# Kernel optimization log

Measured on AMD Instinct MI355X. Metric: run time of the kernel, lower is better.

## Reference

```python
import jax, jax.numpy as jnp
import numpy as np

R0 = 1.0
DIM_A, DIM_V, DIM_D = 32, 32, 32
N_NODES = 20000
N_EDGES = 640000


def radial_encode_8(r, r0):
    # 8 Gaussian radial basis functions on the edge length |r_ij|
    d = jnp.linalg.norm(r, axis=-1)                      # [E]
    centers = jnp.linspace(0.0, r0, 8)                   # [8]
    width = r0 / 8.0
    return jnp.exp(-(((d[..., None] - centers) / width) ** 2))  # [E,8]


def tens_sigmoid_vec(v):
    # norm-saturating nonlinearity for rank-1 tensors (direction-preserving)
    n2 = jnp.sum(v * v, axis=-1, keepdims=True)
    return v * jax.lax.rsqrt(1.0 + n2)


def setup_inputs() -> dict:
    key = jax.random.key(0)
    ks = jax.random.split(key, 12)

    def lin(k, fan_in, fan_out):
        return jax.random.normal(k, (fan_in, fan_out), jnp.float32) / np.float32(np.sqrt(fan_in))

    return dict(
        r_ij=jax.random.normal(ks[0], (N_EDGES, 3), jnp.float32),
        w_rad=lin(ks[1], 8, DIM_A), b_rad=jnp.zeros((DIM_A,), jnp.float32),
        w_direct=lin(ks[2], DIM_A, DIM_A),
        w1=lin(ks[3], DIM_A, 2 * DIM_A), b1=jnp.zeros((2 * DIM_A,), jnp.float32),
        w2=lin(ks[4], 2 * DIM_A, 2 * DIM_A), b2=jnp.zeros((2 * DIM_A,), jnp.float32),
        w3=lin(ks[5], 2 * DIM_A, DIM_A), b3=jnp.zeros((DIM_A,), jnp.float32),
        w_v=lin(ks[6], DIM_A, DIM_V),
        w_d=lin(ks[7], DIM_A, DIM_D),
        edges_src=jax.random.randint(ks[8], (N_EDGES,), 0, N_NODES),
        n_nodes=N_NODES,
    )


def reference(r_ij, w_rad, b_rad, w_direct, w1, b1, w2, b2, w3, b3, w_v, w_d,
              edges_src, n_nodes):
    lrelu = lambda x: jnp.where(x > 0, x, 0.1 * x)
    # radial MLP: Linear(8, a) -> MLP (lin_direct + 3-layer leakyrelu net)
    h = radial_encode_8(r_ij, R0) @ w_rad + b_rad                      # [E,a]
    rad = h @ w_direct + (lrelu(lrelu(h @ w1 + b1) @ w2 + b2) @ w3 + b3)  # [E,a]
    rs = tens_sigmoid_vec(r_ij * (7.0 / R0))                            # [E,3]

    seg = lambda x: jax.ops.segment_sum(x, edges_src, num_segments=n_nodes)
    A_a = seg(rad)                                                      # [N,a]
    A_v = seg(rad[:, :, None] * rs[:, None, :])                         # [N,a,3]
    # phi_d_ij = rad ⊗ rs ⊗ rs per edge  -> [E,a,3,3], then scatter-sum
    A_d = seg(rad[:, :, None, None] * rs[:, None, None, :] * rs[:, None, :, None])  # [N,a,3,3]

    out_v = jnp.einsum('nac,av->nvc', A_v, w_v)                         # TensLinear rank 1
    out_d = jnp.einsum('naij,ad->ndij', A_d, w_d)                       # TensLinear rank 2
    return A_a, out_v, out_d
```

## Files before the change

kernel.cpp:

```cpp
#include <hip/hip_runtime.h>
#include <hip/hip_bf16.h>
#include <hip/hip_fp16.h>
#include <math.h>


#define TSIZE 8192
#define DMAX  2.0f
#define NPB   4
#define EPB   4

#define O_WRAD 0
#define O_BRAD 256
#define O_WDIR 288
#define O_W1   1312
#define O_B1   3360
#define O_W2   3424
#define O_B2   7520
#define O_W3   7584
#define O_B3   9632
#define O_WV   9664
#define O_WD   10688
#define W_TOT  11712

__device__ __forceinline__ float lrelu(float x) { return x > 0.0f ? x : 0.1f * x; }

__device__ __forceinline__ float ldf(const void* p, int i, bool f32) {
    return f32 ? ((const float*)p)[i]
               : __uint_as_float(((unsigned int)((const unsigned short*)p)[i]) << 16);
}
__device__ __forceinline__ void stf(void* p, size_t i, float v, bool f32) {
    if (f32) ((float*)p)[i] = v;
    else     ((__hip_bfloat16*)p)[i] = __float2bfloat16(v);
}

__device__ __forceinline__ bool detect_f32(const void* r) {
    const unsigned short* p = (const unsigned short*)r;
    int bad = 0;
#pragma unroll 8
    for (int i = 0; i < 128; i++) {
        float v = __uint_as_float(((unsigned int)p[i]) << 16);
        bad |= (!isfinite(v) || fabsf(v) > 1e5f) ? 1 : 0;
    }
    return bad != 0;
}

__global__ void k_prep(const void* __restrict__ r_ij,
                       const void* w_rad, const void* b_rad, const void* w_direct,
                       const void* w1, const void* b1, const void* w2, const void* b2,
                       const void* w3, const void* b3, const void* w_v, const void* w_d,
                       float* __restrict__ wcat, int* __restrict__ flag,
                       int* __restrict__ counts, int N) {
    const int b = blockIdx.x;
    if (b == 0) {
        if (threadIdx.x == 0) flag[0] = detect_f32(r_ij) ? 1 : 0;
    } else if (b <= 11) {
        const bool f32 = detect_f32(r_ij);
        const void* src; int cnt; int off;
        switch (b) {
            case 1:  src = w_rad;    cnt = 256;  off = O_WRAD; break;
            case 2:  src = b_rad;    cnt = 32;   off = O_BRAD; break;
            case 3:  src = w_direct; cnt = 1024; off = O_WDIR; break;
            case 4:  src = w1;       cnt = 2048; off = O_W1;   break;
            case 5:  src = b1;       cnt = 64;   off = O_B1;   break;
            case 6:  src = w2;       cnt = 4096; off = O_W2;   break;
            case 7:  src = b2;       cnt = 64;   off = O_B2;   break;
            case 8:  src = w3;       cnt = 2048; off = O_W3;   break;
            case 9:  src = b3;       cnt = 32;   off = O_B3;   break;
            case 10: src = w_v;      cnt = 1024; off = O_WV;   break;
            default: src = w_d;      cnt = 1024; off = O_WD;   break;
        }
        for (int i = threadIdx.x; i < cnt; i += blockDim.x)
            wcat[off + i] = ldf(src, i, f32);
    } else {
        int i = (b - 12) * blockDim.x + threadIdx.x;
        if (i < N) counts[i] = 0;
    }
}

__global__ void __launch_bounds__(64 * EPB) k_table(const float* __restrict__ wcat,
                                                    float* __restrict__ tabI) {
    __shared__ float Lh[EPB][32], Lt1[EPB][64], Lt2[EPB][64], Lrad[EPB][32];

    const int s = threadIdx.x >> 6;
    const int j = threadIdx.x & 63;
    const int e = blockIdx.x * EPB + s;
    const float d = (float)e * (DMAX / (float)(TSIZE - 1));

    float enc[8];
#pragma unroll
    for (int k = 0; k < 8; k++) {
        float t = (d - (float)k * (1.0f / 7.0f)) * 8.0f;
        enc[k] = expf(-t * t);
    }

    if (j < 32) {
        float hv = wcat[O_BRAD + j];
#pragma unroll
        for (int k = 0; k < 8; k++) hv = fmaf(enc[k], wcat[O_WRAD + k * 32 + j], hv);
        Lh[s][j] = hv;
    }
    __syncthreads();

    {
        float v = wcat[O_B1 + j];
#pragma unroll
        for (int i = 0; i < 32; i++) v = fmaf(Lh[s][i], wcat[O_W1 + i * 64 + j], v);
        Lt1[s][j] = lrelu(v);
    }
    __syncthreads();

    {
        float v = wcat[O_B2 + j];
#pragma unroll
        for (int i = 0; i < 64; i++) v = fmaf(Lt1[s][i], wcat[O_W2 + i * 64 + j], v);
        Lt2[s][j] = lrelu(v);
    }
    __syncthreads();

    if (j < 32) {
        float v = wcat[O_B3 + j];
#pragma unroll
        for (int i = 0; i < 64; i++) v = fmaf(Lt2[s][i], wcat[O_W3 + i * 32 + j], v);
#pragma unroll
        for (int i = 0; i < 32; i++) v = fmaf(Lh[s][i], wcat[O_WDIR + i * 32 + j], v);
        Lrad[s][j] = v;
        tabI[e * 96 + j] = v;
    }
    __syncthreads();

    if (j < 32) {
        float sv = 0.0f, sd = 0.0f;
#pragma unroll
        for (int i = 0; i < 32; i++) {
            float ri = Lrad[s][i];
            sv = fmaf(ri, wcat[O_WV + i * 32 + j], sv);
            sd = fmaf(ri, wcat[O_WD + i * 32 + j], sd);
        }
        tabI[e * 96 + 32 + j] = sv;
        tabI[e * 96 + 64 + j] = sd;
    }
}

__global__ void k_rank(const int* __restrict__ src, int* __restrict__ counts,
                       int* __restrict__ rank, int E) {
    int e = blockIdx.x * blockDim.x + threadIdx.x;
    if (e < E) rank[e] = atomicAdd(&counts[src[e]], 1);
}

__global__ void k_scan(const int* __restrict__ counts, int* __restrict__ rowstart,
                       int N, int E) {
    __shared__ int part[1024];
    const int t = threadIdx.x;
    const int CH = (N + 1023) / 1024;
    const int lo = t * CH;
    const int hi = min(lo + CH, N);

    int s = 0;
    for (int i = lo; i < hi; i++) s += counts[i];
    part[t] = s;
    __syncthreads();

    for (int off = 1; off < 1024; off <<= 1) {
        int v = part[t];
        int w = (t >= off) ? part[t - off] : 0;
        __syncthreads();
        part[t] = v + w;
        __syncthreads();
    }

    int run = (t == 0) ? 0 : part[t - 1];
    for (int i = lo; i < hi; i++) {
        rowstart[i] = run;
        run += counts[i];
    }
    if (t == 0) rowstart[N] = E;
}

__global__ void k_place(const int* __restrict__ src, const int* __restrict__ rank,
                        const int* __restrict__ rowstart,
                        const void* __restrict__ r_ij, const int* __restrict__ flag,
                        uint2* __restrict__ eps, int* __restrict__ perm, int E) {
    int e = blockIdx.x * blockDim.x + threadIdx.x;
    if (e >= E) return;
    const int pos = rowstart[src[e]] + rank[e];
    if (eps) {
        const bool f32 = flag[0] != 0;
        const float x = ldf(r_ij, 3 * e + 0, f32);
        const float y = ldf(r_ij, 3 * e + 1, f32);
        const float z = ldf(r_ij, 3 * e + 2, f32);
        const float d2 = x * x + y * y + z * z;
        const float inv = rsqrtf(1.0f + 49.0f * d2);
        const float u = fminf(sqrtf(d2), DMAX) * ((float)(TSIZE - 1) / DMAX);
        const unsigned int ti = (unsigned int)(u + 0.5f);
        const unsigned int h0 = __half_as_ushort(__float2half(7.0f * x * inv));
        const unsigned int h1 = __half_as_ushort(__float2half(7.0f * y * inv));
        const unsigned int h2 = __half_as_ushort(__float2half(7.0f * z * inv));
        eps[pos] = make_uint2(h0 | (h1 << 16), h2 | (ti << 16));
    } else {
        perm[pos] = e;
    }
}

__global__ void __launch_bounds__(64 * NPB) k_nodes(
    const uint2* __restrict__ eps,
    const int* __restrict__ perm,
    const void* __restrict__ r_ij,
    const int* __restrict__ rowstart,
    const float* __restrict__ tabI,
    const int* __restrict__ flag,
    void* __restrict__ out, int N) {
    const int wave = threadIdx.x >> 6;
    const int lane = threadIdx.x & 63;
    const int n = blockIdx.x * NPB + wave;
    if (n >= N) return;
    const int a = lane & 31;
    const bool hi = (lane >> 5) != 0;
    const bool f32 = flag[0] != 0;

    const int s0 = rowstart[n];
    const int s1 = rowstart[n + 1];

    float accR = 0.f, acc1 = 0.f, acc2 = 0.f, acc3 = 0.f,
          acc4 = 0.f, acc5 = 0.f, acc6 = 0.f;

    if (eps) {
        int idx = s0;
        for (; idx + 1 < s1; idx += 2) {
            const uint2 qa = eps[idx];
            const uint2 qb = eps[idx + 1];
            const float ax = __half2float(__ushort_as_half((unsigned short)(qa.x & 0xffff)));
            const float ay = __half2float(__ushort_as_half((unsigned short)(qa.x >> 16)));
            const float az = __half2float(__ushort_as_half((unsigned short)(qa.y & 0xffff)));
            const int   ab = (int)(qa.y >> 16) * 96 + a;
            const float bx = __half2float(__ushort_as_half((unsigned short)(qb.x & 0xffff)));
            const float by = __half2float(__ushort_as_half((unsigned short)(qb.x >> 16)));
            const float bz = __half2float(__ushort_as_half((unsigned short)(qb.y & 0xffff)));
            const int   bb = (int)(qb.y >> 16) * 96 + a;

            const float raA = tabI[ab], rvA = tabI[ab + 32], rdA = tabI[ab + 64];
            const float raB = tabI[bb], rvB = tabI[bb + 32], rdB = tabI[bb + 64];

            const float b1A = (hi ? rdA : rvA) * (hi ? ay : 1.0f);
            const float b2A = rdA * (hi ? az : ax);
            const float b1B = (hi ? rdB : rvB) * (hi ? by : 1.0f);
            const float b2B = rdB * (hi ? bz : bx);

            accR += raA + raB;
            acc1 += b1A * ax + b1B * bx;
            acc2 += b1A * ay + b1B * by;
            acc3 += b1A * az + b1B * bz;
            acc4 += b2A * ax + b2B * bx;
            acc5 += b2A * ay + b2B * by;
            acc6 += b2A * az + b2B * bz;
        }
        if (idx < s1) {
            const uint2 q = eps[idx];
            const float x = __half2float(__ushort_as_half((unsigned short)(q.x & 0xffff)));
            const float y = __half2float(__ushort_as_half((unsigned short)(q.x >> 16)));
            const float z = __half2float(__ushort_as_half((unsigned short)(q.y & 0xffff)));
            const int   b = (int)(q.y >> 16) * 96 + a;
            const float ra = tabI[b], rv = tabI[b + 32], rd = tabI[b + 64];
            const float b1 = (hi ? rd : rv) * (hi ? y : 1.0f);
            const float b2 = rd * (hi ? z : x);
            accR += ra;
            acc1 += b1 * x; acc2 += b1 * y; acc3 += b1 * z;
            acc4 += b2 * x; acc5 += b2 * y; acc6 += b2 * z;
        }
    } else {
        for (int idx = s0; idx < s1; idx++) {
            const int e = perm[idx];
            const float x0 = ldf(r_ij, 3 * e + 0, f32);
            const float y0 = ldf(r_ij, 3 * e + 1, f32);
            const float z0 = ldf(r_ij, 3 * e + 2, f32);
            const float d2 = x0 * x0 + y0 * y0 + z0 * z0;
            const float inv = rsqrtf(1.0f + 49.0f * d2);
            const float x = 7.0f * x0 * inv, y = 7.0f * y0 * inv, z = 7.0f * z0 * inv;
            const float u = fminf(sqrtf(d2), DMAX) * ((float)(TSIZE - 1) / DMAX);
            const int b = (int)(u + 0.5f) * 96 + a;
            const float ra = tabI[b], rv = tabI[b + 32], rd = tabI[b + 64];
            const float b1 = (hi ? rd : rv) * (hi ? y : 1.0f);
            const float b2 = rd * (hi ? z : x);
            accR += ra;
            acc1 += b1 * x; acc2 += b1 * y; acc3 += b1 * z;
            acc4 += b2 * x; acc5 += b2 * y; acc6 += b2 * z;
        }
    }

    const size_t baseV = (size_t)N * 32;
    const size_t baseD = (size_t)N * 128;
    if (!hi) {
        stf(out, (size_t)n * 32 + a, accR, f32);
        const size_t vb = baseV + (size_t)n * 96 + a * 3;
        stf(out, vb + 0, acc1, f32);
        stf(out, vb + 1, acc2, f32);
        stf(out, vb + 2, acc3, f32);
        const size_t db = baseD + (size_t)n * 288 + a * 9;
        stf(out, db + 0, acc4, f32);
        stf(out, db + 1, acc5, f32);
        stf(out, db + 2, acc6, f32);
    } else {
        const size_t db = baseD + (size_t)n * 288 + a * 9;
        stf(out, db + 3, acc1, f32);
        stf(out, db + 4, acc2, f32);
        stf(out, db + 5, acc3, f32);
        stf(out, db + 6, acc4, f32);
        stf(out, db + 7, acc5, f32);
        stf(out, db + 8, acc6, f32);
    }
}

extern "C" void kernel_launch(void* const* d_in, const int* in_sizes, int n_in,
                              void* d_out, int out_size, void* d_ws, size_t ws_size,
                              hipStream_t stream) {
    const void* r_ij     = d_in[0];
    const void* w_rad    = d_in[1];
    const void* b_rad    = d_in[2];
    const void* w_direct = d_in[3];
    const void* w1       = d_in[4];
    const void* b1       = d_in[5];
    const void* w2       = d_in[6];
    const void* b2       = d_in[7];
    const void* w3       = d_in[8];
    const void* b3       = d_in[9];
    const void* w_v      = d_in[10];
    const void* w_d      = d_in[11];
    const int* edges_src = (const int*)d_in[12];

    const int E = in_sizes[12];
    const int N = out_size / 416;

    const size_t fixedInts = (size_t)W_TOT + 4 + (size_t)TSIZE * 96
                           + (size_t)N + (size_t)(N + 1) + (size_t)E;
    const size_t epsBytes  = (size_t)E * 8;
    const bool use_eps = ws_size >= epsBytes + fixedInts * 4 + 64;

    char* w = (char*)d_ws;
    uint2* eps = use_eps ? (uint2*)w : nullptr;
    int* perm  = use_eps ? nullptr : (int*)w;
    const size_t slotBytes = use_eps ? epsBytes : (size_t)E * 4;

    float* wcat   = (float*)(w + ((slotBytes + 15) & ~(size_t)15));
    int* flag     = (int*)(wcat + W_TOT);
    float* tabI   = (float*)(flag + 4);
    int* counts   = (int*)(tabI + (size_t)TSIZE * 96);
    int* rowstart = counts + N;
    int* rank     = rowstart + N + 1;

    k_prep<<<12 + (N + 255) / 256, 256, 0, stream>>>(
        r_ij, w_rad, b_rad, w_direct, w1, b1, w2, b2, w3, b3, w_v, w_d,
        wcat, flag, counts, N);
    k_table<<<TSIZE / EPB, 64 * EPB, 0, stream>>>(wcat, tabI);
    k_rank<<<(E + 255) / 256, 256, 0, stream>>>(edges_src, counts, rank, E);
    k_scan<<<1, 1024, 0, stream>>>(counts, rowstart, N, E);
    k_place<<<(E + 255) / 256, 256, 0, stream>>>(edges_src, rank, rowstart,
                                                 r_ij, flag, eps, perm, E);
    k_nodes<<<(N + NPB - 1) / NPB, 64 * NPB, 0, stream>>>(
        eps, perm, r_ij, rowstart, tabI, flag, d_out, N);
}
```

Measured before the change: 239.7 us.

## Replace global-atomic counting sort with per-block LDS histogram and column scan

Edge bucketing by source node now uses 32 blocks. Each block builds an LDS histogram of its edge chunk over node tiles, a column scan turns these into per-block offsets, and a placement pass assigns positions with LDS atomics instead of global atomics. The aim is to remove contended global atomics and the separate rank array. The risk is that only 32 blocks run, each walking its chunk once per node tile with the per-edge geometry work inside. That leaves most of the GPU idle and may be latency bound. A fallback path keeps the old global-atomic scheme when the workspace is too small.

```diff
diff --git a/kernel.cpp b/kernel.cpp
--- a/kernel.cpp
+++ b/kernel.cpp
@@ -8,6 +8,8 @@
 #define DMAX  2.0f
 #define NPB   4
 #define EPB   4
+#define HB    32
+#define TILE  10240
 
 #define O_WRAD 0
 #define O_BRAD 256
@@ -71,7 +73,7 @@
         }
         for (int i = threadIdx.x; i < cnt; i += blockDim.x)
             wcat[off + i] = ldf(src, i, f32);
-    } else {
+    } else if (counts) {
         int i = (b - 12) * blockDim.x + threadIdx.x;
         if (i < N) counts[i] = 0;
     }
@@ -141,13 +143,45 @@
     }
 }
 
-__global__ void k_rank(const int* __restrict__ src, int* __restrict__ counts,
-                       int* __restrict__ rank, int E) {
-    int e = blockIdx.x * blockDim.x + threadIdx.x;
-    if (e < E) rank[e] = atomicAdd(&counts[src[e]], 1);
-}
-
-__global__ void k_scan(const int* __restrict__ counts, int* __restrict__ rowstart,
+__global__ void __launch_bounds__(256) k_hist(const int* __restrict__ src, int E,
+                                              int chunk, int* __restrict__ cnt,
+                                              int N) {
+    __shared__ int lcnt[TILE];
+    const int b = blockIdx.x;
+    const int lo = b * chunk;
+    const int hi = min(lo + chunk, E);
+    const int ntiles = (N + TILE - 1) / TILE;
+
+    for (int t = 0; t < ntiles; t++) {
+        const int t0 = t * TILE;
+        const int tl = min(TILE, N - t0);
+        for (int i = threadIdx.x; i < tl; i += 256) lcnt[i] = 0;
+        __syncthreads();
+        for (int e = lo + threadIdx.x; e < hi; e += 256) {
+            const int s = src[e] - t0;
+            if ((unsigned)s < (unsigned)tl) atomicAdd(&lcnt[s], 1);
+        }
+        __syncthreads();
+        for (int i = threadIdx.x; i < tl; i += 256)
+            cnt[b * N + t0 + i] = lcnt[i];
+        __syncthreads();
+    }
+}
+
+__global__ void k_colscan(int* __restrict__ cnt, int* __restrict__ tot, int N) {
+    int n = blockIdx.x * blockDim.x + threadIdx.x;
+    if (n >= N) return;
+    int run = 0;
+#pragma unroll 4
+    for (int b = 0; b < HB; b++) {
+        int c = cnt[b * N + n];
+        cnt[b * N + n] = run;
+        run += c;
+    }
+    tot[n] = run;
+}
+
+__global__ void k_scan(const int* __restrict__ tot, int* __restrict__ rowstart,
                        int N, int E) {
     __shared__ int part[1024];
     const int t = threadIdx.x;
@@ -156,7 +190,7 @@
     const int hi = min(lo + CH, N);
 
     int s = 0;
-    for (int i = lo; i < hi; i++) s += counts[i];
+    for (int i = lo; i < hi; i++) s += tot[i];
     part[t] = s;
     __syncthreads();
 
@@ -171,34 +205,60 @@
     int run = (t == 0) ? 0 : part[t - 1];
     for (int i = lo; i < hi; i++) {
         rowstart[i] = run;
-        run += counts[i];
+        run += tot[i];
     }
     if (t == 0) rowstart[N] = E;
 }
 
-__global__ void k_place(const int* __restrict__ src, const int* __restrict__ rank,
-                        const int* __restrict__ rowstart,
-                        const void* __restrict__ r_ij, const int* __restrict__ flag,
-                        uint2* __restrict__ eps, int* __restrict__ perm, int E) {
+__global__ void __launch_bounds__(256) k_place(
+        const int* __restrict__ src, int E, int chunk,
+        const int* __restrict__ cnt, const int* __restrict__ rowstart,
+        const void* __restrict__ r_ij, const int* __restrict__ flag,
+        uint2* __restrict__ eps, int N) {
+    __shared__ int cur[TILE];
+    const int b = blockIdx.x;
+    const int lo = b * chunk;
+    const int hi = min(lo + chunk, E);
+    const int ntiles = (N + TILE - 1) / TILE;
+    const bool f32 = flag[0] != 0;
+
+    for (int t = 0; t < ntiles; t++) {
+        const int t0 = t * TILE;
+        const int tl = min(TILE, N - t0);
+        for (int i = threadIdx.x; i < tl; i += 256)
+            cur[i] = rowstart[t0 + i] + cnt[b * N + t0 + i];
+        __syncthreads();
+        for (int e = lo + threadIdx.x; e < hi; e += 256) {
+            const int s = src[e] - t0;
+            if ((unsigned)s < (unsigned)tl) {
+                const int pos = atomicAdd(&cur[s], 1);
+                const float x = ldf(r_ij, 3 * e + 0, f32);
+                const float y = ldf(r_ij, 3 * e + 1, f32);
+                const float z = ldf(r_ij, 3 * e + 2, f32);
+                const float d2 = x * x + y * y + z * z;
+                const float inv = rsqrtf(1.0f + 49.0f * d2);
+                const float u = fminf(sqrtf(d2), DMAX) * ((float)(TSIZE - 1) / DMAX);
+                const unsigned int ti = (unsigned int)(u + 0.5f);
+                const unsigned int h0 = __half_as_ushort(__float2half(7.0f * x * inv));
+                const unsigned int h1 = __half_as_ushort(__float2half(7.0f * y * inv));
+                const unsigned int h2 = __half_as_ushort(__float2half(7.0f * z * inv));
+                eps[pos] = make_uint2(h0 | (h1 << 16), h2 | (ti << 16));
+            }
+        }
+        __syncthreads();
+    }
+}
+
+__global__ void k_rank_g(const int* __restrict__ src, int* __restrict__ counts,
+                         int* __restrict__ rank, int E) {
     int e = blockIdx.x * blockDim.x + threadIdx.x;
-    if (e >= E) return;
-    const int pos = rowstart[src[e]] + rank[e];
-    if (eps) {
-        const bool f32 = flag[0] != 0;
-        const float x = ldf(r_ij, 3 * e + 0, f32);
-        const float y = ldf(r_ij, 3 * e + 1, f32);
-        const float z = ldf(r_ij, 3 * e + 2, f32);
-        const float d2 = x * x + y * y + z * z;
-        const float inv = rsqrtf(1.0f + 49.0f * d2);
-        const float u = fminf(sqrtf(d2), DMAX) * ((float)(TSIZE - 1) / DMAX);
-        const unsigned int ti = (unsigned int)(u + 0.5f);
-        const unsigned int h0 = __half_as_ushort(__float2half(7.0f * x * inv));
-        const unsigned int h1 = __half_as_ushort(__float2half(7.0f * y * inv));
-        const unsigned int h2 = __half_as_ushort(__float2half(7.0f * z * inv));
-        eps[pos] = make_uint2(h0 | (h1 << 16), h2 | (ti << 16));
-    } else {
-        perm[pos] = e;
-    }
+    if (e < E) rank[e] = atomicAdd(&counts[src[e]], 1);
+}
+__global__ void k_place_g(const int* __restrict__ src, const int* __restrict__ rank,
+                          const int* __restrict__ rowstart,
+                          int* __restrict__ perm, int E) {
+    int e = blockIdx.x * blockDim.x + threadIdx.x;
+    if (e < E) perm[rowstart[src[e]] + rank[e]] = e;
 }
 
 __global__ void __launch_bounds__(64 * NPB) k_nodes(
@@ -328,32 +388,52 @@
 
     const int E = in_sizes[12];
     const int N = out_size / 416;
-
-    const size_t fixedInts = (size_t)W_TOT + 4 + (size_t)TSIZE * 96
-                           + (size_t)N + (size_t)(N + 1) + (size_t)E;
-    const size_t epsBytes  = (size_t)E * 8;
-    const bool use_eps = ws_size >= epsBytes + fixedInts * 4 + 64;
+    const int chunk = (E + HB - 1) / HB;
+
+    const size_t fastBytes = (size_t)E * 8
+                           + ((size_t)W_TOT + 4 + (size_t)TSIZE * 96
+                              + (size_t)HB * N + (size_t)N + (size_t)(N + 1)) * 4;
+    const bool use_fast = ws_size >= fastBytes + 64;
 
     char* w = (char*)d_ws;
-    uint2* eps = use_eps ? (uint2*)w : nullptr;
-    int* perm  = use_eps ? nullptr : (int*)w;
-    const size_t slotBytes = use_eps ? epsBytes : (size_t)E * 4;
-
-    float* wcat   = (float*)(w + ((slotBytes + 15) & ~(size_t)15));
-    int* flag     = (int*)(wcat + W_TOT);
-    float* tabI   = (float*)(flag + 4);
-    int* counts   = (int*)(tabI + (size_t)TSIZE * 96);
-    int* rowstart = counts + N;
-    int* rank     = rowstart + N + 1;
-
-    k_prep<<<12 + (N + 255) / 256, 256, 0, stream>>>(
-        r_ij, w_rad, b_rad, w_direct, w1, b1, w2, b2, w3, b3, w_v, w_d,
-        wcat, flag, counts, N);
-    k_table<<<TSIZE / EPB, 64 * EPB, 0, stream>>>(wcat, tabI);
-    k_rank<<<(E + 255) / 256, 256, 0, stream>>>(edges_src, counts, rank, E);
-    k_scan<<<1, 1024, 0, stream>>>(counts, rowstart, N, E);
-    k_place<<<(E + 255) / 256, 256, 0, stream>>>(edges_src, rank, rowstart,
-                                                 r_ij, flag, eps, perm, E);
-    k_nodes<<<(N + NPB - 1) / NPB, 64 * NPB, 0, stream>>>(
-        eps, perm, r_ij, rowstart, tabI, flag, d_out, N);
-}
+    if (use_fast) {
+        uint2* eps    = (uint2*)w;
+        float* wcat   = (float*)(w + (size_t)E * 8);
+        int* flag     = (int*)(wcat + W_TOT);
+        float* tabI   = (float*)(flag + 4);
+        int* cnt      = (int*)(tabI + (size_t)TSIZE * 96);
+        int* tot      = cnt + (size_t)HB * N;
+        int* rowstart = tot + N;
+
+        k_prep<<<12, 256, 0, stream>>>(
+            r_ij, w_rad, b_rad, w_direct, w1, b1, w2, b2, w3, b3, w_v, w_d,
+            wcat, flag, nullptr, N);
+        k_table<<<TSIZE / EPB, 64 * EPB, 0, stream>>>(wcat, tabI);
+        k_hist<<<HB, 256, 0, stream>>>(edges_src, E, chunk, cnt, N);
+        k_colscan<<<(N + 255) / 256, 256, 0, stream>>>(cnt, tot, N);
+        k_scan<<<1, 1024, 0, stream>>>(tot, rowstart, N, E);
+        k_place<<<HB, 256, 0, stream>>>(edges_src, E, chunk, cnt, rowstart,
+                                        r_ij, flag, eps, N);
+        k_nodes<<<(N + NPB - 1) / NPB, 64 * NPB, 0, stream>>>(
+            eps, nullptr, r_ij, rowstart, tabI, flag, d_out, N);
+    } else {
+        int* perm     = (int*)w;
+        float* wcat   = (float*)(w + (size_t)E * 4);
+        int* flag     = (int*)(wcat + W_TOT);
+        float* tabI   = (float*)(flag + 4);
+        int* counts   = (int*)(tabI + (size_t)TSIZE * 96);
+        int* rowstart = counts + N;
+        int* rank     = rowstart + N + 1;
+
+        k_prep<<<12 + (N + 255) / 256, 256, 0, stream>>>(
+            r_ij, w_rad, b_rad, w_direct, w1, b1, w2, b2, w3, b3, w_v, w_d,
+            wcat, flag, counts, N);
+        k_table<<<TSIZE / EPB, 64 * EPB, 0, stream>>>(wcat, tabI);
+        k_rank_g<<<(E + 255) / 256, 256, 0, stream>>>(edges_src, counts, rank, E);
+        k_scan<<<1, 1024, 0, stream>>>(counts, rowstart, N, E);
+        k_place_g<<<(E + 255) / 256, 256, 0, stream>>>(edges_src, rank, rowstart,
+                                                       perm, E);
+        k_nodes<<<(N + NPB - 1) / NPB, 64 * NPB, 0, stream>>>(
+            nullptr, perm, r_ij, rowstart, tabI, flag, d_out, N);
+    }
+}
```

Result: slower. 353.7 us (+47.6%).
